# Kernel optimization log

Measured on AMD Instinct MI355X. Metric: run time of the kernel, lower is better.

The kernel has to match this reference:

```python
import jax, jax.numpy as jnp
import numpy as np

R = 10  # num_relations
NUM_GRAPHS = 64


def rgcn_layer(x, W, root, b, src, dst, etype):
    # x: [N, Din], W: [R, Din, H], root: [Din, H], b: [H]
    N = x.shape[0]
    H = W.shape[-1]
    # per-relation transform of all nodes: [R, N, H]
    h_all = jnp.einsum('nd,rdh->rnh', x, W)
    # gather transformed source features per edge by its relation: [E, H]
    msg = h_all[etype, src]
    # mean-aggregate per (dst, relation) pair, then sum over relations (PyG RGCNConv semantics)
    key = dst * R + etype
    sums = jax.ops.segment_sum(msg, key, num_segments=N * R)  # [N*R, H]
    cnt = jax.ops.segment_sum(jnp.ones((etype.shape[0],), x.dtype), key, num_segments=N * R)
    agg = (sums.reshape(N, R, H) / jnp.clip(cnt.reshape(N, R, 1), 1.0, None)).sum(axis=1)
    return agg + x @ root + b


def setup_inputs() -> dict:
    key = jax.random.key(0)
    ks = jax.random.split(key, 12)
    N, E, DIN, H = 100000, 3200000, 128, 64
    x = jax.random.normal(ks[0], (N, DIN), dtype=jnp.float32)
    edge_index = jax.random.randint(ks[1], (2, E), 0, N, dtype=jnp.int64)
    edge_type = jax.random.randint(ks[2], (E,), 0, R, dtype=jnp.int64)
    batch = jnp.sort(jax.random.randint(ks[3], (N,), 0, NUM_GRAPHS, dtype=jnp.int64))
    s1 = 1.0 / np.sqrt(DIN)
    s2 = 1.0 / np.sqrt(H)
    W1 = jax.random.uniform(ks[4], (R, DIN, H), jnp.float32, -s1, s1)
    root1 = jax.random.uniform(ks[5], (DIN, H), jnp.float32, -s1, s1)
    b1 = jnp.zeros((H,), jnp.float32)
    W2 = jax.random.uniform(ks[6], (R, H, H), jnp.float32, -s2, s2)
    root2 = jax.random.uniform(ks[7], (H, H), jnp.float32, -s2, s2)
    b2 = jnp.zeros((H,), jnp.float32)
    cls_w = jax.random.uniform(ks[8], (H, 1), jnp.float32, -s2, s2)
    cls_b = jnp.zeros((1,), jnp.float32)
    return {"x": x, "edge_index": edge_index, "edge_type": edge_type, "batch": batch,
            "W1": W1, "root1": root1, "b1": b1, "W2": W2, "root2": root2, "b2": b2,
            "cls_w": cls_w, "cls_b": cls_b}


def reference(x, edge_index, edge_type, batch, W1, root1, b1, W2, root2, b2, cls_w, cls_b):
    src, dst = edge_index[0], edge_index[1]
    h = jax.nn.relu(rgcn_layer(x, W1, root1, b1, src, dst, edge_type))   # dropout = identity (eval)
    h = jax.nn.relu(rgcn_layer(h, W2, root2, b2, src, dst, edge_type))
    # global mean pool per graph
    sums = jax.ops.segment_sum(h, batch, num_segments=NUM_GRAPHS)        # [G, H]
    cnt = jax.ops.segment_sum(jnp.ones((h.shape[0],), h.dtype), batch, num_segments=NUM_GRAPHS)
    pooled = sums / jnp.clip(cnt[:, None], 1.0, None)
    out = pooled @ cls_w + cls_b                                          # [G, 1]
    return out.reshape(-1)
```

## Files before the change

### kernel.cpp

```cpp
#include <hip/hip_runtime.h>

#define R_REL 10
#define HD 64
#define BSH 8
#define KPB (256 * R_REL)
#define SORT_CAP 12288

typedef __attribute__((ext_vector_type(8))) short short8;
typedef __attribute__((ext_vector_type(4))) float floatx4;
typedef __attribute__((ext_vector_type(8))) unsigned short ushort8;

__device__ inline unsigned short f32_to_bf16_rne(float f) {
    unsigned int u = __float_as_uint(f);
    unsigned int r = (u + 0x7FFFu + ((u >> 16) & 1u)) >> 16;
    return (unsigned short)r;
}
__device__ inline float bf16_to_f32(unsigned short h) {
    return __uint_as_float(((unsigned int)h) << 16);
}
__device__ inline float bf16lo(unsigned int u) { return __uint_as_float(u << 16); }
__device__ inline float bf16hi(unsigned int u) { return __uint_as_float(u & 0xFFFF0000u); }

__device__ __forceinline__ void gload_lds16(const unsigned short* g, unsigned short* l) {
    __builtin_amdgcn_global_load_lds(
        (const __attribute__((address_space(1))) unsigned int*)g,
        (__attribute__((address_space(3))) unsigned int*)l, 16, 0, 0);
}

#define BAR_VMCNT(N)                                              \
    do {                                                          \
        asm volatile("s_waitcnt vmcnt(" #N ")" ::: "memory");     \
        __builtin_amdgcn_sched_barrier(0);                        \
        __builtin_amdgcn_s_barrier();                             \
        __builtin_amdgcn_sched_barrier(0);                        \
    } while (0)

__global__ __launch_bounds__(256) void bhist_kernel(const int* __restrict__ dst,
                                                    int* __restrict__ bcnt, int E) {
    __shared__ int l[512];
    int t = threadIdx.x;
    l[t] = 0; l[t + 256] = 0;
    __syncthreads();
    int e0 = blockIdx.x * 4096;
    for (int i = t; i < 4096; i += 256) {
        int e = e0 + i;
        if (e < E) atomicAdd(&l[dst[e] >> BSH], 1);
    }
    __syncthreads();
    if (l[t]) atomicAdd(&bcnt[t], l[t]);
    if (l[t + 256]) atomicAdd(&bcnt[t + 256], l[t + 256]);
}

__global__ void bscan_kernel(const int* __restrict__ bcnt, int* __restrict__ boff,
                             int* __restrict__ gcursor, int NBK, int E) {
    int t = threadIdx.x;
    int v = (t < NBK) ? bcnt[t] : 0;
    __shared__ int tmp[512];
    tmp[t] = v;
    __syncthreads();
    for (int off = 1; off < 512; off <<= 1) {
        int u = (t >= off) ? tmp[t - off] : 0;
        __syncthreads();
        tmp[t] += u;
        __syncthreads();
    }
    int excl = tmp[t] - v;
    if (t < NBK) { boff[t] = excl; gcursor[t] = excl; }
    if (t == 0) boff[NBK] = E;
}

__global__ __launch_bounds__(256) void bscatter_kernel(const int* __restrict__ src,
                                                       const int* __restrict__ dst,
                                                       const int* __restrict__ et,
                                                       int* __restrict__ gcursor,
                                                       unsigned int* __restrict__ staged,
                                                       int E) {
    __shared__ int lcnt[512];
    __shared__ int lstart[512];
    __shared__ int lbase[512];
    __shared__ int tmp[256];
    __shared__ unsigned int lbuf[4096];
    __shared__ unsigned short lbkt[4096];
    int t = threadIdx.x;
    int e0 = blockIdx.x * 4096;
    int nthis = min(4096, E - e0);
    lcnt[t] = 0; lcnt[t + 256] = 0;
    __syncthreads();
    for (int i = t; i < nthis; i += 256) atomicAdd(&lcnt[dst[e0 + i] >> BSH], 1);
    __syncthreads();
    int c0 = lcnt[2 * t], c1 = lcnt[2 * t + 1];
    int ps = c0 + c1;
    tmp[t] = ps;
    __syncthreads();
    for (int off = 1; off < 256; off <<= 1) {
        int u = (t >= off) ? tmp[t - off] : 0;
        __syncthreads();
        tmp[t] += u;
        __syncthreads();
    }
    int ex = tmp[t] - ps;
    lstart[2 * t] = ex; lstart[2 * t + 1] = ex + c0;
    lbase[2 * t]     = (c0 > 0) ? atomicAdd(&gcursor[2 * t], c0) : 0;
    lbase[2 * t + 1] = (c1 > 0) ? atomicAdd(&gcursor[2 * t + 1], c1) : 0;
    __syncthreads();
    lcnt[t] = 0; lcnt[t + 256] = 0;
    __syncthreads();
    for (int i = t; i < nthis; i += 256) {
        int dd = dst[e0 + i];
        int bk = dd >> BSH;
        int lk = (dd & ((1 << BSH) - 1)) * R_REL + et[e0 + i];
        unsigned int p = ((unsigned int)lk << 17) | (unsigned int)src[e0 + i];
        int pos = lstart[bk] + atomicAdd(&lcnt[bk], 1);
        lbuf[pos] = p; lbkt[pos] = (unsigned short)bk;
    }
    __syncthreads();
    for (int i = t; i < nthis; i += 256) {
        int bk = lbkt[i];
        staged[lbase[bk] + i - lstart[bk]] = lbuf[i];
    }
}

__global__ __launch_bounds__(256) void sortfill_kernel(const unsigned int* __restrict__ staged,
                                                       const int* __restrict__ boff,
                                                       int* __restrict__ dcnt,
                                                       int2* __restrict__ edata,
                                                       int N, int Ntot) {
    __shared__ int hist[KPB];
    __shared__ float wkey[KPB];
    __shared__ int part[256];
    __shared__ int lsrc[SORT_CAP];
    __shared__ unsigned short lkey[SORT_CAP];
    int t = threadIdx.x, b = blockIdx.x;
    int s0 = boff[b], s1 = boff[b + 1];
#pragma unroll
    for (int j = 0; j < KPB / 256; ++j) hist[t + j * 256] = 0;
    __syncthreads();
    for (int i = s0 + t; i < s1; i += 256)
        atomicAdd(&hist[staged[i] >> 17], 1);
    __syncthreads();
    int base = t * (KPB / 256);
    int c[KPB / 256];
    int s = 0;
#pragma unroll
    for (int j = 0; j < KPB / 256; ++j) {
        c[j] = hist[base + j]; s += c[j];
        wkey[base + j] = 1.0f / fmaxf((float)c[j], 1.0f);
    }
    int dglob = b * 256 + t;
    if (dglob < Ntot) dcnt[dglob] = s;
    part[t] = s;
    __syncthreads();
    for (int off = 1; off < 256; off <<= 1) {
        int u = (t >= off) ? part[t - off] : 0;
        __syncthreads();
        part[t] += u;
        __syncthreads();
    }
    int run = part[t] - s;
#pragma unroll
    for (int j = 0; j < KPB / 256; ++j) { hist[base + j] = run; run += c[j]; }
    __syncthreads();
    for (int i = s0 + t; i < s1; i += 256) {
        unsigned int p = staged[i];
        int lk = p >> 17;
        int pos = atomicAdd(&hist[lk], 1);
        if (pos < SORT_CAP) { lsrc[pos] = (int)(p & 0x1FFFFu); lkey[pos] = (unsigned short)lk; }
        else {
            int rel = lk % R_REL;
            edata[s0 + pos] = make_int2(rel * N + (int)(p & 0x1FFFFu), __float_as_int(wkey[lk]));
        }
    }
    __syncthreads();
    int m = min(s1 - s0, SORT_CAP);
    for (int j = t; j < m; j += 256) {
        int lk = lkey[j];
        int rel = lk % R_REL;
        edata[s0 + j] = make_int2(rel * N + lsrc[j], __float_as_int(wkey[lk]));
    }
}

__global__ void scan1_kernel(const int* __restrict__ cnt, int* __restrict__ bsum, int M) {
    int b = blockIdx.x, tid = threadIdx.x;
    int base = b * 1024 + tid * 4;
    int s = 0;
#pragma unroll
    for (int j = 0; j < 4; ++j) { int i = base + j; if (i < M) s += cnt[i]; }
    for (int off = 32; off > 0; off >>= 1) s += __shfl_down(s, off);
    __shared__ int wsum[4];
    int lane = tid & 63, wid = tid >> 6;
    if (lane == 0) wsum[wid] = s;
    __syncthreads();
    if (tid == 0) bsum[b] = wsum[0] + wsum[1] + wsum[2] + wsum[3];
}

__global__ void scan2_kernel(const int* __restrict__ bsum, int* __restrict__ boff, int NB) {
    int tid = threadIdx.x;
    int lane = tid & 63, wid = tid >> 6;
    int v = (tid < NB) ? bsum[tid] : 0;
    int x = v;
    for (int off = 1; off < 64; off <<= 1) { int u = __shfl_up(x, off); if (lane >= off) x += u; }
    __shared__ int wsum[16];
    if (lane == 63) wsum[wid] = x;
    __syncthreads();
    int woff = 0;
    for (int w = 0; w < wid; ++w) woff += wsum[w];
    if (tid < NB) boff[tid] = x + woff - v;
}

__global__ void scan3_kernel(const int* __restrict__ cnt, const int* __restrict__ boff,
                             int* __restrict__ rowptr, int M) {
    int b = blockIdx.x, tid = threadIdx.x;
    int base = b * 1024 + tid * 4;
    int c[4]; int s = 0;
#pragma unroll
    for (int j = 0; j < 4; ++j) { int i = base + j; c[j] = (i < M) ? cnt[i] : 0; s += c[j]; }
    int lane = tid & 63, wid = tid >> 6;
    int x = s;
    for (int off = 1; off < 64; off <<= 1) { int u = __shfl_up(x, off); if (lane >= off) x += u; }
    __shared__ int wsum[4];
    if (lane == 63) wsum[wid] = x;
    __syncthreads();
    int woff = 0;
    for (int w = 0; w < wid; ++w) woff += wsum[w];
    int run = boff[b] + x + woff - s;
#pragma unroll
    for (int j = 0; j < 4; ++j) {
        int i = base + j;
        if (i < M) {
            rowptr[i] = run; run += c[j];
            if (i == M - 1) rowptr[M] = run;
        }
    }
}

__global__ void split_kernel(const float* __restrict__ src, unsigned short* __restrict__ hi,
                             unsigned short* __restrict__ lo, int n) {
    int i = blockIdx.x * 256 + threadIdx.x;
    if (i < n) {
        float v = src[i];
        unsigned short h = f32_to_bf16_rne(v);
        hi[i] = h;
        lo[i] = f32_to_bf16_rne(v - bf16_to_f32(h));
    }
}

__global__ void wsplit_kernel(const float* __restrict__ W, const float* __restrict__ root,
                              unsigned short* __restrict__ hi, unsigned short* __restrict__ lo,
                              int K) {
    int idx = blockIdx.x * 256 + threadIdx.x;
    int total = (R_REL + 1) * HD * K;
    if (idx >= total) return;
    int rel = idx / (HD * K);
    int rem = idx - rel * HD * K;
    int n = rem / K, k = rem - n * K;
    float v = (rel < R_REL) ? W[((size_t)rel * K + k) * HD + n] : root[(size_t)k * HD + n];
    unsigned short h = f32_to_bf16_rne(v);
    int ks = k ^ ((n & 7) << 3);
    int widx = rel * HD * K + n * K + ks;
    hi[widx] = h;
    lo[widx] = f32_to_bf16_rne(v - bf16_to_f32(h));
}

template <int K>
__global__ __launch_bounds__(512, 4)
void gemm_mfma(const unsigned short* __restrict__ Xhi,
               const unsigned short* __restrict__ Xlo,
               const unsigned short* __restrict__ Wthi,
               const unsigned short* __restrict__ Wtlo,
               unsigned short* __restrict__ hout,
               float* __restrict__ fout, int N) {
    constexpr int NS = K / 32;
    constexpr int TILE_SH = HD * K;
    constexpr int TILEB = TILE_SH * 2;
    constexpr int HALFC = K / 8;
    __shared__ unsigned short wlds[4 * TILE_SH];
    const int tid = threadIdx.x;
    const int w = tid >> 6, lane = tid & 63;
    const int quad = lane >> 4, l16 = lane & 15;
    const int wr = w >> 2, wc = w & 3;
    const int n0 = blockIdx.x * 128;
    const int nodeA = n0 + wc * 32 + l16;
    const int nodeB = nodeA + 16;
    const bool vA = nodeA < N, vB = nodeB < N;

    short8 Xh[2][NS], Xl[2][NS];
#pragma unroll
    for (int s = 0; s < NS; ++s) {
        short8 z;
#pragma unroll
        for (int q = 0; q < 8; ++q) z[q] = 0;
        Xh[0][s] = z; Xl[0][s] = z; Xh[1][s] = z; Xl[1][s] = z;
        if (vA) {
            Xh[0][s] = *(const short8*)(Xhi + (size_t)nodeA * K + s * 32 + quad * 8);
            Xl[0][s] = *(const short8*)(Xlo + (size_t)nodeA * K + s * 32 + quad * 8);
        }
        if (vB) {
            Xh[1][s] = *(const short8*)(Xhi + (size_t)nodeB * K + s * 32 + quad * 8);
            Xl[1][s] = *(const short8*)(Xlo + (size_t)nodeB * K + s * 32 + quad * 8);
        }
    }

    auto stage = [&](int rel, int b) {
        const unsigned short* hsrc = Wthi + (size_t)rel * TILE_SH;
        const unsigned short* lsrc = Wtlo + (size_t)rel * TILE_SH;
        unsigned short* dst0 = wlds + b * 2 * TILE_SH;
#pragma unroll
        for (int j = 0; j < NS; ++j) {
            int q = j * 8 + w;
            const unsigned short* src = (q < HALFC) ? (hsrc + q * 512)
                                                    : (lsrc + (q - HALFC) * 512);
            gload_lds16(src + lane * 8, dst0 + q * 512);
        }
    };

    stage(0, 0);
    BAR_VMCNT(0);

    const int swzb = (l16 & 7) << 4;
    const size_t NHD = (size_t)N * HD;

#pragma unroll
    for (int c = 0; c <= R_REL; ++c) {
        const int cur = c & 1;
        if (c < R_REL) stage(c + 1, cur ^ 1);
        const char* wb = (const char*)(wlds + cur * 2 * TILE_SH);
        floatx4 acc[2][2];
#pragma unroll
        for (int mt = 0; mt < 2; ++mt) {
            floatx4 z = {0.f, 0.f, 0.f, 0.f};
            acc[mt][0] = z; acc[mt][1] = z;
        }
#pragma unroll
        for (int s = 0; s < NS; ++s) {
            const int koffb = ((s * 32 + quad * 8) * 2) ^ swzb;
#pragma unroll
            for (int mt = 0; mt < 2; ++mt) {
                const int rowb = (wr * 32 + mt * 16 + l16) * (K * 2);
                short8 Wh = *(const short8*)(wb + rowb + koffb);
                short8 Wl = *(const short8*)(wb + TILEB + rowb + koffb);
#pragma unroll
                for (int nh = 0; nh < 2; ++nh) {
                    acc[mt][nh] = __builtin_amdgcn_mfma_f32_16x16x32_bf16(Wh, Xh[nh][s], acc[mt][nh], 0, 0, 0);
                    acc[mt][nh] = __builtin_amdgcn_mfma_f32_16x16x32_bf16(Wh, Xl[nh][s], acc[mt][nh], 0, 0, 0);
                    acc[mt][nh] = __builtin_amdgcn_mfma_f32_16x16x32_bf16(Wl, Xh[nh][s], acc[mt][nh], 0, 0, 0);
                }
            }
        }
        if (c < R_REL) {
#pragma unroll
            for (int mt = 0; mt < 2; ++mt) {
#pragma unroll
                for (int nh = 0; nh < 2; ++nh) {
                    int node = (nh == 0) ? nodeA : nodeB;
                    if (nh == 0 ? vA : vB) {
                        unsigned int d0 = (unsigned int)f32_to_bf16_rne(acc[mt][nh][0]) |
                                          ((unsigned int)f32_to_bf16_rne(acc[mt][nh][1]) << 16);
                        unsigned int d1 = (unsigned int)f32_to_bf16_rne(acc[mt][nh][2]) |
                                          ((unsigned int)f32_to_bf16_rne(acc[mt][nh][3]) << 16);
                        *(uint2*)(hout + (size_t)c * NHD + (size_t)node * HD +
                                  wr * 32 + mt * 16 + quad * 4) = make_uint2(d0, d1);
                    }
                }
            }
        } else {
#pragma unroll
            for (int mt = 0; mt < 2; ++mt) {
#pragma unroll
                for (int nh = 0; nh < 2; ++nh) {
                    int node = (nh == 0) ? nodeA : nodeB;
                    if (nh == 0 ? vA : vB)
                        *(floatx4*)(fout + (size_t)node * HD + wr * 32 + mt * 16 + quad * 4) =
                            acc[mt][nh];
                }
            }
        }
        if (c < R_REL) {
            BAR_VMCNT(4);
        }
    }
}

__global__ __launch_bounds__(256) void agg_kernel(const unsigned short* __restrict__ hc,
                                                  const int* __restrict__ rowptr,
                                                  const int2* __restrict__ edata,
                                                  float* __restrict__ acc, int N) {
    int gid = blockIdx.x * 256 + threadIdx.x;
    int d = gid >> 6;
    if (d >= N) return;
    int lane = threadIdx.x & 63;
    int quarter = lane >> 4, l16 = lane & 15;
    int e0 = rowptr[d], e1 = rowptr[d + 1];
    int ne = e1 - e0;
    if (ne == 0) return;
    float s0 = 0.f, s1 = 0.f, s2 = 0.f, s3 = 0.f;
    for (int rb = 0; rb < ne; rb += 64) {
        int nthis = min(64, ne - rb);
        int2 ed = make_int2(0, 0);
        if (lane < nthis) ed = edata[e0 + rb + lane];
        int off = ed.x << 6;
        float wv = __int_as_float(ed.y);
        for (int j = 0; j < nthis; j += 8) {
            int   oa = __shfl(off, j + quarter);
            float wa = __shfl(wv,  j + quarter);
            int   ob = __shfl(off, j + 4 + quarter);
            float wb = __shfl(wv,  j + 4 + quarter);
            uint2 da = *(const uint2*)(hc + oa + l16 * 4);
            uint2 db = *(const uint2*)(hc + ob + l16 * 4);
            s0 += wa * bf16lo(da.x); s1 += wa * bf16hi(da.x);
            s2 += wa * bf16lo(da.y); s3 += wa * bf16hi(da.y);
            s0 += wb * bf16lo(db.x); s1 += wb * bf16hi(db.x);
            s2 += wb * bf16lo(db.y); s3 += wb * bf16hi(db.y);
        }
    }
    s0 += __shfl_xor(s0, 16); s1 += __shfl_xor(s1, 16);
    s2 += __shfl_xor(s2, 16); s3 += __shfl_xor(s3, 16);
    s0 += __shfl_xor(s0, 32); s1 += __shfl_xor(s1, 32);
    s2 += __shfl_xor(s2, 32); s3 += __shfl_xor(s3, 32);
    if (lane < 16) {
        float4* ap = (float4*)(acc + (size_t)d * HD + l16 * 4);
        float4 a = *ap;
        a.x += s0; a.y += s1; a.z += s2; a.w += s3;
        *ap = a;
    }
}

__global__ void fin1_kernel(const float* __restrict__ acc, const float* __restrict__ bias,
                            unsigned short* __restrict__ hi, unsigned short* __restrict__ lo,
                            int NH) {
    int i = blockIdx.x * 256 + threadIdx.x;
    if (i < NH) {
        float v = fmaxf(acc[i] + bias[i & (HD - 1)], 0.f);
        unsigned short h = f32_to_bf16_rne(v);
        hi[i] = h;
        lo[i] = f32_to_bf16_rne(v - bf16_to_f32(h));
    }
}

__global__ __launch_bounds__(256) void pool_kernel(const float* __restrict__ acc,
                                                   const float* __restrict__ bias,
                                                   const int* __restrict__ batch,
                                                   float* __restrict__ pooled,
                                                   float* __restrict__ gcnt, int N) {
    int w = blockIdx.x * 4 + (threadIdx.x >> 6);
    int lane = threadIdx.x & 63;
    int base = w * 64;
    if (base >= N) return;
    int nn = min(64, N - base);
    float b = bias[lane];
    int g_l = (base + lane < N) ? batch[base + lane] : -1;
    int g_first = __shfl(g_l, 0);
    int g_last = __shfl(g_l, nn - 1);
    if (nn == 64 && g_first == g_last) {
        float p0 = 0.f, p1 = 0.f, p2 = 0.f, p3 = 0.f;
#pragma unroll
        for (int i = 0; i < 64; i += 4) {
            p0 += fmaxf(acc[(size_t)(base + i + 0) * HD + lane] + b, 0.f);
            p1 += fmaxf(acc[(size_t)(base + i + 1) * HD + lane] + b, 0.f);
            p2 += fmaxf(acc[(size_t)(base + i + 2) * HD + lane] + b, 0.f);
            p3 += fmaxf(acc[(size_t)(base + i + 3) * HD + lane] + b, 0.f);
        }
        atomicAdd(&pooled[g_first * HD + lane], (p0 + p1) + (p2 + p3));
        if (lane == 0) atomicAdd(&gcnt[g_first], 64.f);
    } else {
        int cur = g_first; float s = 0.f; int cnt = 0;
        for (int i = 0; i < nn; ++i) {
            int g = __shfl(g_l, i);
            if (g != cur) {
                atomicAdd(&pooled[cur * HD + lane], s);
                if (lane == 0) atomicAdd(&gcnt[cur], (float)cnt);
                cur = g; s = 0.f; cnt = 0;
            }
            s += fmaxf(acc[(size_t)(base + i) * HD + lane] + b, 0.f);
            cnt++;
        }
        atomicAdd(&pooled[cur * HD + lane], s);
        if (lane == 0) atomicAdd(&gcnt[cur], (float)cnt);
    }
}

__global__ void cls_kernel(const float* __restrict__ pooled, const float* __restrict__ gcnt,
                           const float* __restrict__ cls_w, const float* __restrict__ cls_b,
                           float* __restrict__ out) {
    int g = threadIdx.x;
    float invc = 1.0f / fmaxf(gcnt[g], 1.0f);
    float acc = 0.f;
    for (int j = 0; j < 64; ++j) acc += pooled[g * 64 + j] * cls_w[j];
    out[g] = acc * invc + cls_b[0];
}

extern "C" void kernel_launch(void* const* d_in, const int* in_sizes, int n_in,
                              void* d_out, int out_size, void* d_ws, size_t ws_size,
                              hipStream_t stream) {
    const float* x     = (const float*)d_in[0];
    const int*   eidx  = (const int*)d_in[1];
    const int*   et    = (const int*)d_in[2];
    const int*   batch = (const int*)d_in[3];
    const float* W1    = (const float*)d_in[4];
    const float* root1 = (const float*)d_in[5];
    const float* b1    = (const float*)d_in[6];
    const float* W2    = (const float*)d_in[7];
    const float* root2 = (const float*)d_in[8];
    const float* b2    = (const float*)d_in[9];
    const float* cls_w = (const float*)d_in[10];
    const float* cls_b = (const float*)d_in[11];

    const int N = in_sizes[3];
    const int E = in_sizes[2];
    const int NB = (N + 1023) / 1024;
    const int NBK = (N + (1 << BSH) - 1) >> BSH;
    const int* srcp = eidx;
    const int* dstp = eidx + E;

    char* ws = (char*)d_ws;
    size_t off = 0;
    auto alloc = [&](size_t bytes) -> void* {
        void* p = ws + off;
        off = (off + bytes + 255) & ~(size_t)255;
        return p;
    };
    unsigned short* Xhi  = (unsigned short*)alloc((size_t)N * 128 * 2);
    unsigned short* Xlo  = (unsigned short*)alloc((size_t)N * 128 * 2);
    float*          accb = (float*)alloc((size_t)N * HD * 4);
    unsigned short* Wt1hi = (unsigned short*)alloc((size_t)(R_REL + 1) * HD * 128 * 2);
    unsigned short* Wt1lo = (unsigned short*)alloc((size_t)(R_REL + 1) * HD * 128 * 2);
    unsigned short* Wt2hi = (unsigned short*)alloc((size_t)(R_REL + 1) * HD * HD * 2);
    unsigned short* Wt2lo = (unsigned short*)alloc((size_t)(R_REL + 1) * HD * HD * 2);
    int2*  edata  = (int2*)alloc((size_t)E * 8);
    int*   rowptr = (int*)alloc((size_t)(N + 1) * 4);
    int*   dcnt   = (int*)alloc((size_t)N * 4);
    int*   bsum   = (int*)alloc((size_t)NB * 4);
    int*   bofs   = (int*)alloc((size_t)NB * 4);
    int*   bcnt   = (int*)alloc(512 * 4);
    int*   bboff  = (int*)alloc(513 * 4);
    int*   gcur   = (int*)alloc(512 * 4);
    float* pooled = (float*)alloc((size_t)(64 * HD + 64) * 4);
    float* gcnt   = pooled + 64 * HD;
    unsigned short* h_chunk = (unsigned short*)alloc((size_t)R_REL * N * HD * 2);

    unsigned int* staged = (unsigned int*)Xhi;
    unsigned short* H1hi = Xhi;
    unsigned short* H1lo = Xlo;

    hipMemsetAsync(bcnt, 0, 512 * 4, stream);
    hipMemsetAsync(pooled, 0, (size_t)(64 * HD + 64) * 4, stream);

    int nchunks = (E + 4095) / 4096;
    bhist_kernel<<<nchunks, 256, 0, stream>>>(dstp, bcnt, E);
    bscan_kernel<<<1, 512, 0, stream>>>(bcnt, bboff, gcur, NBK, E);
    bscatter_kernel<<<nchunks, 256, 0, stream>>>(srcp, dstp, et, gcur, staged, E);
    sortfill_kernel<<<NBK, 256, 0, stream>>>(staged, bboff, dcnt, edata, N, N);
    scan1_kernel<<<NB, 256, 0, stream>>>(dcnt, bsum, N);
    scan2_kernel<<<1, 1024, 0, stream>>>(bsum, bofs, NB);
    scan3_kernel<<<NB, 256, 0, stream>>>(dcnt, bofs, rowptr, N);

    int NK = N * 128;
    split_kernel<<<(NK + 255) / 256, 256, 0, stream>>>(x, Xhi, Xlo, NK);
    int tw1 = (R_REL + 1) * HD * 128, tw2 = (R_REL + 1) * HD * HD;
    wsplit_kernel<<<(tw1 + 255) / 256, 256, 0, stream>>>(W1, root1, Wt1hi, Wt1lo, 128);
    wsplit_kernel<<<(tw2 + 255) / 256, 256, 0, stream>>>(W2, root2, Wt2hi, Wt2lo, HD);

    const int gemmBlocks = (N + 127) / 128;
    const int aggBlocks  = (int)(((size_t)N * 64 + 255) / 256);
    const int NH = N * HD;

    gemm_mfma<128><<<gemmBlocks, 512, 0, stream>>>(Xhi, Xlo, Wt1hi, Wt1lo, h_chunk, accb, N);
    agg_kernel<<<aggBlocks, 256, 0, stream>>>(h_chunk, rowptr, edata, accb, N);
    fin1_kernel<<<(NH + 255) / 256, 256, 0, stream>>>(accb, b1, H1hi, H1lo, NH);

    gemm_mfma<64><<<gemmBlocks, 512, 0, stream>>>(H1hi, H1lo, Wt2hi, Wt2lo, h_chunk, accb, N);
    agg_kernel<<<aggBlocks, 256, 0, stream>>>(h_chunk, rowptr, edata, accb, N);

    int poolWaves = (N + 63) / 64;
    pool_kernel<<<(poolWaves + 3) / 4, 256, 0, stream>>>(accb, b2, batch, pooled, gcnt, N);
    cls_kernel<<<1, 64, 0, stream>>>(pooled, gcnt, cls_w, cls_b, (float*)d_out);
}
```

Before: 596.9 us.

## Drop weight low-bf16 split and halve GEMM block to 256 threads

```diff
diff --git a/kernel.cpp b/kernel.cpp
--- a/kernel.cpp
+++ b/kernel.cpp
@@ -245,8 +245,7 @@
 }
 
 __global__ void wsplit_kernel(const float* __restrict__ W, const float* __restrict__ root,
-                              unsigned short* __restrict__ hi, unsigned short* __restrict__ lo,
-                              int K) {
+                              unsigned short* __restrict__ hi, int K) {
     int idx = blockIdx.x * 256 + threadIdx.x;
     int total = (R_REL + 1) * HD * K;
     if (idx >= total) return;
@@ -254,34 +253,29 @@
     int rem = idx - rel * HD * K;
     int n = rem / K, k = rem - n * K;
     float v = (rel < R_REL) ? W[((size_t)rel * K + k) * HD + n] : root[(size_t)k * HD + n];
-    unsigned short h = f32_to_bf16_rne(v);
     int ks = k ^ ((n & 7) << 3);
-    int widx = rel * HD * K + n * K + ks;
-    hi[widx] = h;
-    lo[widx] = f32_to_bf16_rne(v - bf16_to_f32(h));
+    hi[rel * HD * K + n * K + ks] = f32_to_bf16_rne(v);
 }
 
 template <int K>
-__global__ __launch_bounds__(512, 4)
+__global__ __launch_bounds__(256, 5)
 void gemm_mfma(const unsigned short* __restrict__ Xhi,
                const unsigned short* __restrict__ Xlo,
                const unsigned short* __restrict__ Wthi,
-               const unsigned short* __restrict__ Wtlo,
                unsigned short* __restrict__ hout,
                float* __restrict__ fout, int N) {
     constexpr int NS = K / 32;
     constexpr int TILE_SH = HD * K;
-    constexpr int TILEB = TILE_SH * 2;
-    constexpr int HALFC = K / 8;
-    __shared__ unsigned short wlds[4 * TILE_SH];
+    __shared__ unsigned short wlds[2 * TILE_SH];
     const int tid = threadIdx.x;
     const int w = tid >> 6, lane = tid & 63;
     const int quad = lane >> 4, l16 = lane & 15;
-    const int wr = w >> 2, wc = w & 3;
-    const int n0 = blockIdx.x * 128;
+    const int wr = w >> 1, wc = w & 1;
+    const int n0 = blockIdx.x * 64;
     const int nodeA = n0 + wc * 32 + l16;
     const int nodeB = nodeA + 16;
     const bool vA = nodeA < N, vB = nodeB < N;
+    const bool full = (n0 + 64 <= N);
 
     short8 Xh[2][NS], Xl[2][NS];
 #pragma unroll
@@ -302,14 +296,11 @@
 
     auto stage = [&](int rel, int b) {
         const unsigned short* hsrc = Wthi + (size_t)rel * TILE_SH;
-        const unsigned short* lsrc = Wtlo + (size_t)rel * TILE_SH;
-        unsigned short* dst0 = wlds + b * 2 * TILE_SH;
+        unsigned short* dst0 = wlds + b * TILE_SH;
 #pragma unroll
         for (int j = 0; j < NS; ++j) {
-            int q = j * 8 + w;
-            const unsigned short* src = (q < HALFC) ? (hsrc + q * 512)
-                                                    : (lsrc + (q - HALFC) * 512);
-            gload_lds16(src + lane * 8, dst0 + q * 512);
+            int q = j * 4 + w;
+            gload_lds16(hsrc + q * 512 + lane * 8, dst0 + q * 512);
         }
     };
 
@@ -323,7 +314,7 @@
     for (int c = 0; c <= R_REL; ++c) {
         const int cur = c & 1;
         if (c < R_REL) stage(c + 1, cur ^ 1);
-        const char* wb = (const char*)(wlds + cur * 2 * TILE_SH);
+        const char* wb = (const char*)(wlds + cur * TILE_SH);
         floatx4 acc[2][2];
 #pragma unroll
         for (int mt = 0; mt < 2; ++mt) {
@@ -337,12 +328,10 @@
             for (int mt = 0; mt < 2; ++mt) {
                 const int rowb = (wr * 32 + mt * 16 + l16) * (K * 2);
                 short8 Wh = *(const short8*)(wb + rowb + koffb);
-                short8 Wl = *(const short8*)(wb + TILEB + rowb + koffb);
 #pragma unroll
                 for (int nh = 0; nh < 2; ++nh) {
                     acc[mt][nh] = __builtin_amdgcn_mfma_f32_16x16x32_bf16(Wh, Xh[nh][s], acc[mt][nh], 0, 0, 0);
                     acc[mt][nh] = __builtin_amdgcn_mfma_f32_16x16x32_bf16(Wh, Xl[nh][s], acc[mt][nh], 0, 0, 0);
-                    acc[mt][nh] = __builtin_amdgcn_mfma_f32_16x16x32_bf16(Wl, Xh[nh][s], acc[mt][nh], 0, 0, 0);
                 }
             }
         }
@@ -375,7 +364,7 @@
             }
         }
         if (c < R_REL) {
-            BAR_VMCNT(4);
+            if (full) BAR_VMCNT(4); else BAR_VMCNT(0);
         }
     }
 }
@@ -522,9 +511,7 @@
     unsigned short* Xlo  = (unsigned short*)alloc((size_t)N * 128 * 2);
     float*          accb = (float*)alloc((size_t)N * HD * 4);
     unsigned short* Wt1hi = (unsigned short*)alloc((size_t)(R_REL + 1) * HD * 128 * 2);
-    unsigned short* Wt1lo = (unsigned short*)alloc((size_t)(R_REL + 1) * HD * 128 * 2);
     unsigned short* Wt2hi = (unsigned short*)alloc((size_t)(R_REL + 1) * HD * HD * 2);
-    unsigned short* Wt2lo = (unsigned short*)alloc((size_t)(R_REL + 1) * HD * HD * 2);
     int2*  edata  = (int2*)alloc((size_t)E * 8);
     int*   rowptr = (int*)alloc((size_t)(N + 1) * 4);
     int*   dcnt   = (int*)alloc((size_t)N * 4);
@@ -556,18 +543,18 @@
     int NK = N * 128;
     split_kernel<<<(NK + 255) / 256, 256, 0, stream>>>(x, Xhi, Xlo, NK);
     int tw1 = (R_REL + 1) * HD * 128, tw2 = (R_REL + 1) * HD * HD;
-    wsplit_kernel<<<(tw1 + 255) / 256, 256, 0, stream>>>(W1, root1, Wt1hi, Wt1lo, 128);
-    wsplit_kernel<<<(tw2 + 255) / 256, 256, 0, stream>>>(W2, root2, Wt2hi, Wt2lo, HD);
-
-    const int gemmBlocks = (N + 127) / 128;
+    wsplit_kernel<<<(tw1 + 255) / 256, 256, 0, stream>>>(W1, root1, Wt1hi, 128);
+    wsplit_kernel<<<(tw2 + 255) / 256, 256, 0, stream>>>(W2, root2, Wt2hi, HD);
+
+    const int gemmBlocks = (N + 63) / 64;
     const int aggBlocks  = (int)(((size_t)N * 64 + 255) / 256);
     const int NH = N * HD;
 
-    gemm_mfma<128><<<gemmBlocks, 512, 0, stream>>>(Xhi, Xlo, Wt1hi, Wt1lo, h_chunk, accb, N);
+    gemm_mfma<128><<<gemmBlocks, 256, 0, stream>>>(Xhi, Xlo, Wt1hi, h_chunk, accb, N);
     agg_kernel<<<aggBlocks, 256, 0, stream>>>(h_chunk, rowptr, edata, accb, N);
     fin1_kernel<<<(NH + 255) / 256, 256, 0, stream>>>(accb, b1, H1hi, H1lo, NH);
 
-    gemm_mfma<64><<<gemmBlocks, 512, 0, stream>>>(H1hi, H1lo, Wt2hi, Wt2lo, h_chunk, accb, N);
+    gemm_mfma<64><<<gemmBlocks, 256, 0, stream>>>(H1hi, H1lo, Wt2hi, h_chunk, accb, N);
     agg_kernel<<<aggBlocks, 256, 0, stream>>>(h_chunk, rowptr, edata, accb, N);
 
     int poolWaves = (N + 63) / 64;
```

After: 600.8 us. Within noise of the previous version (+0.6%).
